# Optimization experiments

Hardware: AMD Instinct MI355X
Metric: run time of the kernel (lower is better)

The kernel has to match this reference:

```python
import jax, jax.numpy as jnp
import numpy as np

B, N, C = 8, 2048, 512
CR = C // 8  # reduced channels = int(channels * 1/8) = 64


def setup_inputs() -> dict:
    key = jax.random.key(0)
    ks = jax.random.split(key, 8)
    s = 0.02
    return {
        "x": jax.random.normal(ks[0], (B, N, C), dtype=jnp.float32),
        "Wk": jax.random.normal(ks[1], (CR, C), dtype=jnp.float32) * s,
        "bk": jax.random.normal(ks[2], (CR,), dtype=jnp.float32) * s,
        "Wv": jax.random.normal(ks[3], (CR, C), dtype=jnp.float32) * s,
        "bv": jax.random.normal(ks[4], (CR,), dtype=jnp.float32) * s,
        "Wq": jax.random.normal(ks[5], (C, C), dtype=jnp.float32) * s,
        "bq": jax.random.normal(ks[6], (C,), dtype=jnp.float32) * s,
        "gamma": jax.random.normal(ks[7], (1,), dtype=jnp.float32),
    }


def reference(x, Wk, bk, Wv, bv, Wq, bq, gamma):
    # x: [B, N, C]; flat_x in torch is x.transpose(1,2) -> [B, C, N]
    fx = jnp.transpose(x, (0, 2, 1))  # [B, C, N]
    # conv1d kernel_size=1 == channel projection
    k = jnp.einsum('oc,bcn->bno', Wk, fx) + bk            # [B, N, CR] (already transposed)
    v = jnp.einsum('oc,bcn->bon', Wv, fx) + bv[:, None]   # [B, CR, N]
    kv = jnp.einsum('bnc,bcm->bnm', k, v)                 # [B, N, N]
    att = jax.nn.softmax(kv, axis=1)                      # softmax over dim=1 as in torch
    q = jnp.einsum('oc,bcn->bon', Wq, fx) + bq[:, None]   # [B, C, N]
    refined = jnp.einsum('bcn,bnm->bcm', q, att)          # [B, C, N]
    refined = jnp.transpose(refined, (0, 2, 1))           # back to [B, N, C]
    return gamma * refined + x
```

## Files before the change

kernel.cpp:

```cpp
#include <hip/hip_runtime.h>

typedef __attribute__((ext_vector_type(4))) float f32x4;
typedef __attribute__((ext_vector_type(8))) __bf16 bf16x8;
typedef __attribute__((ext_vector_type(8))) unsigned short u16x8;

__device__ __forceinline__ unsigned short f2bf(float f) {
  unsigned u = __builtin_bit_cast(unsigned, f);
  u += 0x7fffu + ((u >> 16) & 1u);
  return (unsigned short)(u >> 16);
}
__device__ __forceinline__ unsigned pack2bf(float lo, float hi) {
  return (unsigned)f2bf(lo) | ((unsigned)f2bf(hi) << 16);
}
__device__ __forceinline__ u16x8 cvt8(float4 a, float4 b) {
  u16x8 h;
  h[0] = f2bf(a.x); h[1] = f2bf(a.y); h[2] = f2bf(a.z); h[3] = f2bf(a.w);
  h[4] = f2bf(b.x); h[5] = f2bf(b.y); h[6] = f2bf(b.z); h[7] = f2bf(b.w);
  return h;
}
__device__ __forceinline__ bf16x8 frag_at(const unsigned short* p) {
  return *reinterpret_cast<const bf16x8*>(p);
}
__device__ __forceinline__ f32x4 mfma16(bf16x8 a, bf16x8 b, f32x4 c) {
  return __builtin_amdgcn_mfma_f32_16x16x32_bf16(a, b, c, 0, 0, 0);
}

__global__ __launch_bounds__(512, 2) void proj_all_kernel(
    const float* __restrict__ x,
    const float* __restrict__ Wk, const float* __restrict__ bk,
    const float* __restrict__ Wv, const float* __restrict__ bv,
    const float* __restrict__ Wq, const float* __restrict__ bq,
    unsigned short* __restrict__ kbf, unsigned short* __restrict__ vtbf,
    unsigned short* __restrict__ qt) {
  __shared__ unsigned short As[256][72];
  __shared__ unsigned short Bs[128][72];
  const int t = threadIdx.x;
  const int w = t >> 6, lane = t & 63, lr = lane & 15, lg = lane >> 4;

  if (blockIdx.x < 128) {
    const int tok0 = blockIdx.x * 128;
    const int tr = w & 3, oh = w >> 2;
    f32x4 acc[2][4];
#pragma unroll
    for (int a = 0; a < 2; ++a)
#pragma unroll
      for (int c = 0; c < 4; ++c) acc[a][c] = (f32x4){0.f, 0.f, 0.f, 0.f};

    for (int kk = 0; kk < 8; ++kk) {
      const int k0 = kk * 64;
      {
        int row = t >> 2, q = t & 3;
        const float4* src = reinterpret_cast<const float4*>(
            x + (size_t)(tok0 + row) * 512 + k0 + q * 16);
        float4 f0 = src[0], f1 = src[1], f2 = src[2], f3 = src[3];
        *reinterpret_cast<u16x8*>(&As[row][q * 16])     = cvt8(f0, f1);
        *reinterpret_cast<u16x8*>(&As[row][q * 16 + 8]) = cvt8(f2, f3);
      }
      {
        int row = t >> 2, q = t & 3;
        const float* wsrc = (row < 64) ? (Wk + (size_t)row * 512)
                                       : (Wv + (size_t)(row - 64) * 512);
        const float4* src = reinterpret_cast<const float4*>(wsrc + k0 + q * 16);
        float4 f0 = src[0], f1 = src[1], f2 = src[2], f3 = src[3];
        *reinterpret_cast<u16x8*>(&Bs[row][q * 16])     = cvt8(f0, f1);
        *reinterpret_cast<u16x8*>(&Bs[row][q * 16 + 8]) = cvt8(f2, f3);
      }
      __syncthreads();
#pragma unroll
      for (int s = 0; s < 2; ++s) {
        bf16x8 af[2];
#pragma unroll
        for (int tb = 0; tb < 2; ++tb)
          af[tb] = frag_at(&As[tr * 32 + tb * 16 + lr][s * 32 + lg * 8]);
#pragma unroll
        for (int ob = 0; ob < 4; ++ob) {
          bf16x8 bfr = frag_at(&Bs[oh * 64 + ob * 16 + lr][s * 32 + lg * 8]);
#pragma unroll
          for (int tb = 0; tb < 2; ++tb)
            acc[tb][ob] = mfma16(af[tb], bfr, acc[tb][ob]);
        }
      }
      __syncthreads();
    }
#pragma unroll
    for (int ob = 0; ob < 4; ++ob) {
      const int o = oh * 64 + ob * 16 + lr;
      const float bias = (o < 64) ? bk[o] : bv[o - 64];
#pragma unroll
      for (int tb = 0; tb < 2; ++tb)
#pragma unroll
        for (int i = 0; i < 4; ++i) {
          const int token = tok0 + tr * 32 + tb * 16 + lg * 4 + i;
          const unsigned short hv = f2bf(acc[tb][ob][i] + bias);
          if (o < 64) kbf[(size_t)token * 64 + o] = hv;
          else        vtbf[(size_t)token * 64 + (o - 64)] = hv;
        }
    }
  } else {
    const int bi = blockIdx.x - 128;
    const int b = bi & 7, r = bi >> 3, ot = r >> 4, ntl = r & 15;
    const int o0 = ot * 256, n0 = ntl * 128;
    const int orr = w & 3, nh = w >> 2;
    f32x4 acc[4][4];
#pragma unroll
    for (int a = 0; a < 4; ++a)
#pragma unroll
      for (int c = 0; c < 4; ++c) acc[a][c] = (f32x4){0.f, 0.f, 0.f, 0.f};

    for (int kk = 0; kk < 8; ++kk) {
      const int k0 = kk * 64;
      {
        int row = t >> 1, h = t & 1;
        const float4* src = reinterpret_cast<const float4*>(
            Wq + (size_t)(o0 + row) * 512 + k0 + h * 32);
        float4 f0 = src[0], f1 = src[1];
        *reinterpret_cast<u16x8*>(&As[row][h * 32]) = cvt8(f0, f1);
        float4 f2 = src[2], f3 = src[3];
        *reinterpret_cast<u16x8*>(&As[row][h * 32 + 8]) = cvt8(f2, f3);
        float4 f4 = src[4], f5 = src[5];
        *reinterpret_cast<u16x8*>(&As[row][h * 32 + 16]) = cvt8(f4, f5);
        float4 f6 = src[6], f7 = src[7];
        *reinterpret_cast<u16x8*>(&As[row][h * 32 + 24]) = cvt8(f6, f7);
      }
      {
        int row = t >> 2, q = t & 3;
        const float4* src = reinterpret_cast<const float4*>(
            x + ((size_t)b * 2048 + n0 + row) * 512 + k0 + q * 16);
        float4 f0 = src[0], f1 = src[1], f2 = src[2], f3 = src[3];
        *reinterpret_cast<u16x8*>(&Bs[row][q * 16])     = cvt8(f0, f1);
        *reinterpret_cast<u16x8*>(&Bs[row][q * 16 + 8]) = cvt8(f2, f3);
      }
      __syncthreads();
#pragma unroll
      for (int s = 0; s < 2; ++s) {
        bf16x8 bfr[4];
#pragma unroll
        for (int nb = 0; nb < 4; ++nb)
          bfr[nb] = frag_at(&Bs[nh * 64 + nb * 16 + lr][s * 32 + lg * 8]);
#pragma unroll
        for (int ob = 0; ob < 4; ++ob) {
          bf16x8 af = frag_at(&As[orr * 64 + ob * 16 + lr][s * 32 + lg * 8]);
#pragma unroll
          for (int nb = 0; nb < 4; ++nb)
            acc[ob][nb] = mfma16(af, bfr[nb], acc[ob][nb]);
        }
      }
      __syncthreads();
    }
#pragma unroll
    for (int ob = 0; ob < 4; ++ob)
#pragma unroll
      for (int i = 0; i < 4; ++i) {
        const int o = o0 + orr * 64 + ob * 16 + lg * 4 + i;
        const float bias = bq[o];
#pragma unroll
        for (int nb = 0; nb < 4; ++nb) {
          const int n = n0 + nh * 64 + nb * 16 + lr;
          qt[((size_t)b * 512 + o) * 2048 + n] = f2bf(acc[ob][nb][i] + bias);
        }
      }
  }
}

__global__ __launch_bounds__(256, 2) void attn_kernel(
    const float* __restrict__ x, const unsigned short* __restrict__ kbf,
    const unsigned short* __restrict__ vtbf, const unsigned short* __restrict__ qt,
    const float* __restrict__ g, float* __restrict__ out) {
  __shared__ unsigned short p_lds[2][64][72];
  __shared__ float dsum_lds[64];
  const int t = threadIdx.x;
  const int b = blockIdx.x & 7;
  const int rest = blockIdx.x >> 3;
  const int mt = rest >> 1, ch = rest & 1;
  const int m0 = mt * 64;
  const int w = t >> 6, lane = t & 63, lr = lane & 15, lg = lane >> 4;

  const unsigned short* kbase = kbf + (size_t)b * 2048 * 64;
  const unsigned short* vrow =
      vtbf + (size_t)(b * 2048 + m0 + w * 16 + lr) * 64;
  const bf16x8 qf0 = frag_at(vrow + lg * 8);
  const bf16x8 qf1 = frag_at(vrow + 32 + lg * 8);
  const unsigned short* qtb = qt + ((size_t)b * 512 + ch * 256 + w * 64) * 2048;

  f32x4 acc[4][4];
#pragma unroll
  for (int mc = 0; mc < 4; ++mc)
#pragma unroll
    for (int cb = 0; cb < 4; ++cb) acc[mc][cb] = (f32x4){0.f, 0.f, 0.f, 0.f};
  float dsum = 0.f;

  bf16x8 kf[4][2], bfr[4][2];
#pragma unroll
  for (int nb = 0; nb < 4; ++nb) {
    const unsigned short* krow = kbase + (size_t)(nb * 16 + lr) * 64;
    kf[nb][0] = frag_at(krow + lg * 8);
    kf[nb][1] = frag_at(krow + 32 + lg * 8);
  }
#pragma unroll
  for (int cb = 0; cb < 4; ++cb) {
    const unsigned short* qrow = qtb + (size_t)(cb * 16 + lr) * 2048;
    bfr[cb][0] = frag_at(qrow + lg * 8);
    bfr[cb][1] = frag_at(qrow + 32 + lg * 8);
  }

  for (int nt = 0; nt < 32; ++nt) {
    const int buf = nt & 1;
    const int nn = ((nt + 1) & 31) * 64;

    f32x4 sacc[4];
#pragma unroll
    for (int nb = 0; nb < 4; ++nb) {
      sacc[nb] = (f32x4){0.f, 0.f, 0.f, 0.f};
      sacc[nb] = mfma16(kf[nb][0], qf0, sacc[nb]);
      sacc[nb] = mfma16(kf[nb][1], qf1, sacc[nb]);
    }
#pragma unroll
    for (int nb = 0; nb < 4; ++nb) {
      const unsigned short* krow = kbase + (size_t)(nn + nb * 16 + lr) * 64;
      kf[nb][0] = frag_at(krow + lg * 8);
      kf[nb][1] = frag_at(krow + 32 + lg * 8);
    }
#pragma unroll
    for (int nb = 0; nb < 4; ++nb) {
      float e0 = __expf(sacc[nb][0]);
      float e1 = __expf(sacc[nb][1]);
      float e2 = __expf(sacc[nb][2]);
      float e3 = __expf(sacc[nb][3]);
      dsum += (e0 + e1) + (e2 + e3);
      uint2 pk;
      pk.x = pack2bf(e0, e1);
      pk.y = pack2bf(e2, e3);
      *reinterpret_cast<uint2*>(&p_lds[buf][w * 16 + lr][nb * 16 + lg * 4]) = pk;
    }
    __syncthreads();

#pragma unroll
    for (int mc = 0; mc < 4; ++mc) {
      bf16x8 pf0 = frag_at(&p_lds[buf][mc * 16 + lr][lg * 8]);
      bf16x8 pf1 = frag_at(&p_lds[buf][mc * 16 + lr][32 + lg * 8]);
#pragma unroll
      for (int cb = 0; cb < 4; ++cb) {
        acc[mc][cb] = mfma16(pf0, bfr[cb][0], acc[mc][cb]);
        acc[mc][cb] = mfma16(pf1, bfr[cb][1], acc[mc][cb]);
      }
    }
#pragma unroll
    for (int cb = 0; cb < 4; ++cb) {
      const unsigned short* qrow = qtb + (size_t)(cb * 16 + lr) * 2048 + nn;
      bfr[cb][0] = frag_at(qrow + lg * 8);
      bfr[cb][1] = frag_at(qrow + 32 + lg * 8);
    }
  }

  dsum += __shfl_xor(dsum, 16);
  dsum += __shfl_xor(dsum, 32);
  if (lane < 16) dsum_lds[w * 16 + lane] = dsum;
  __syncthreads();

  const float gamma = g[0];
#pragma unroll
  for (int mc = 0; mc < 4; ++mc) {
#pragma unroll
    for (int i = 0; i < 4; ++i) {
      const int mrow = mc * 16 + lg * 4 + i;
      const float s = gamma / dsum_lds[mrow];
      const size_t base =
          ((size_t)b * 2048 + m0 + mrow) * 512 + ch * 256 + w * 64;
#pragma unroll
      for (int cb = 0; cb < 4; ++cb) {
        const size_t idx = base + cb * 16 + lr;
        out[idx] = acc[mc][cb][i] * s + x[idx];
      }
    }
  }
}

extern "C" void kernel_launch(void* const* d_in, const int* in_sizes, int n_in,
                              void* d_out, int out_size, void* d_ws, size_t ws_size,
                              hipStream_t stream) {
  const float* x  = (const float*)d_in[0];
  const float* Wk = (const float*)d_in[1];
  const float* bk = (const float*)d_in[2];
  const float* Wv = (const float*)d_in[3];
  const float* bv = (const float*)d_in[4];
  const float* Wq = (const float*)d_in[5];
  const float* bq = (const float*)d_in[6];
  const float* g  = (const float*)d_in[7];
  float* out = (float*)d_out;

  char* ws = (char*)d_ws;
  unsigned short* kbf  = (unsigned short*)(ws);
  unsigned short* vtbf = (unsigned short*)(ws + 2097152);
  unsigned short* qt   = (unsigned short*)(ws + 4194304);

  hipLaunchKernelGGL(proj_all_kernel, dim3(384), dim3(512), 0, stream,
                     x, Wk, bk, Wv, bv, Wq, bq, kbf, vtbf, qt);
  hipLaunchKernelGGL(attn_kernel, dim3(512), dim3(256), 0, stream,
                     x, kbf, vtbf, qt, g, out);
}
```

Before: 250.1 us.

## Shrink projection and attention tiles to double grid size and raise occupancy

```diff
diff --git a/kernel.cpp b/kernel.cpp
--- a/kernel.cpp
+++ b/kernel.cpp
@@ -1,22 +1,18 @@
 #include <hip/hip_runtime.h>
 
 typedef __attribute__((ext_vector_type(4))) float f32x4;
+typedef __attribute__((ext_vector_type(4))) __bf16 bf16x4;
 typedef __attribute__((ext_vector_type(8))) __bf16 bf16x8;
 typedef __attribute__((ext_vector_type(8))) unsigned short u16x8;
 
 __device__ __forceinline__ unsigned short f2bf(float f) {
-  unsigned u = __builtin_bit_cast(unsigned, f);
-  u += 0x7fffu + ((u >> 16) & 1u);
-  return (unsigned short)(u >> 16);
-}
-__device__ __forceinline__ unsigned pack2bf(float lo, float hi) {
-  return (unsigned)f2bf(lo) | ((unsigned)f2bf(hi) << 16);
+  __bf16 h = (__bf16)f;
+  return __builtin_bit_cast(unsigned short, h);
 }
 __device__ __forceinline__ u16x8 cvt8(float4 a, float4 b) {
-  u16x8 h;
-  h[0] = f2bf(a.x); h[1] = f2bf(a.y); h[2] = f2bf(a.z); h[3] = f2bf(a.w);
-  h[4] = f2bf(b.x); h[5] = f2bf(b.y); h[6] = f2bf(b.z); h[7] = f2bf(b.w);
-  return h;
+  bf16x8 h = {(__bf16)a.x, (__bf16)a.y, (__bf16)a.z, (__bf16)a.w,
+              (__bf16)b.x, (__bf16)b.y, (__bf16)b.z, (__bf16)b.w};
+  return __builtin_bit_cast(u16x8, h);
 }
 __device__ __forceinline__ bf16x8 frag_at(const unsigned short* p) {
   return *reinterpret_cast<const bf16x8*>(p);
@@ -25,73 +21,67 @@
   return __builtin_amdgcn_mfma_f32_16x16x32_bf16(a, b, c, 0, 0, 0);
 }
 
-__global__ __launch_bounds__(512, 2) void proj_all_kernel(
+__global__ __launch_bounds__(512, 4) void proj_all_kernel(
     const float* __restrict__ x,
     const float* __restrict__ Wk, const float* __restrict__ bk,
     const float* __restrict__ Wv, const float* __restrict__ bv,
     const float* __restrict__ Wq, const float* __restrict__ bq,
     unsigned short* __restrict__ kbf, unsigned short* __restrict__ vtbf,
     unsigned short* __restrict__ qt) {
-  __shared__ unsigned short As[256][72];
+  __shared__ unsigned short As[128][72];
   __shared__ unsigned short Bs[128][72];
   const int t = threadIdx.x;
   const int w = t >> 6, lane = t & 63, lr = lane & 15, lg = lane >> 4;
+  const int wr = w >> 2, wc = w & 3;
+  const int srow = t >> 2, sq = t & 3;
+
+  f32x4 acc[4][2];
+#pragma unroll
+  for (int a = 0; a < 4; ++a)
+#pragma unroll
+    for (int c = 0; c < 2; ++c) acc[a][c] = (f32x4){0.f, 0.f, 0.f, 0.f};
 
   if (blockIdx.x < 128) {
     const int tok0 = blockIdx.x * 128;
-    const int tr = w & 3, oh = w >> 2;
-    f32x4 acc[2][4];
-#pragma unroll
-    for (int a = 0; a < 2; ++a)
-#pragma unroll
-      for (int c = 0; c < 4; ++c) acc[a][c] = (f32x4){0.f, 0.f, 0.f, 0.f};
-
+    const float* wrow = (srow < 64) ? (Wk + (size_t)srow * 512)
+                                    : (Wv + (size_t)(srow - 64) * 512);
     for (int kk = 0; kk < 8; ++kk) {
       const int k0 = kk * 64;
       {
-        int row = t >> 2, q = t & 3;
-        const float4* src = reinterpret_cast<const float4*>(
-            x + (size_t)(tok0 + row) * 512 + k0 + q * 16);
-        float4 f0 = src[0], f1 = src[1], f2 = src[2], f3 = src[3];
-        *reinterpret_cast<u16x8*>(&As[row][q * 16])     = cvt8(f0, f1);
-        *reinterpret_cast<u16x8*>(&As[row][q * 16 + 8]) = cvt8(f2, f3);
-      }
-      {
-        int row = t >> 2, q = t & 3;
-        const float* wsrc = (row < 64) ? (Wk + (size_t)row * 512)
-                                       : (Wv + (size_t)(row - 64) * 512);
-        const float4* src = reinterpret_cast<const float4*>(wsrc + k0 + q * 16);
-        float4 f0 = src[0], f1 = src[1], f2 = src[2], f3 = src[3];
-        *reinterpret_cast<u16x8*>(&Bs[row][q * 16])     = cvt8(f0, f1);
-        *reinterpret_cast<u16x8*>(&Bs[row][q * 16 + 8]) = cvt8(f2, f3);
+        const float4* sa = reinterpret_cast<const float4*>(
+            x + (size_t)(tok0 + srow) * 512 + k0 + sq * 16);
+        float4 a0 = sa[0], a1 = sa[1], a2 = sa[2], a3 = sa[3];
+        *reinterpret_cast<u16x8*>(&As[srow][sq * 16])     = cvt8(a0, a1);
+        *reinterpret_cast<u16x8*>(&As[srow][sq * 16 + 8]) = cvt8(a2, a3);
+        const float4* sb = reinterpret_cast<const float4*>(wrow + k0 + sq * 16);
+        float4 b0 = sb[0], b1 = sb[1], b2 = sb[2], b3 = sb[3];
+        *reinterpret_cast<u16x8*>(&Bs[srow][sq * 16])     = cvt8(b0, b1);
+        *reinterpret_cast<u16x8*>(&Bs[srow][sq * 16 + 8]) = cvt8(b2, b3);
       }
       __syncthreads();
 #pragma unroll
       for (int s = 0; s < 2; ++s) {
-        bf16x8 af[2];
-#pragma unroll
-        for (int tb = 0; tb < 2; ++tb)
-          af[tb] = frag_at(&As[tr * 32 + tb * 16 + lr][s * 32 + lg * 8]);
-#pragma unroll
-        for (int ob = 0; ob < 4; ++ob) {
-          bf16x8 bfr = frag_at(&Bs[oh * 64 + ob * 16 + lr][s * 32 + lg * 8]);
-#pragma unroll
-          for (int tb = 0; tb < 2; ++tb)
-            acc[tb][ob] = mfma16(af[tb], bfr, acc[tb][ob]);
-        }
-      }
-      __syncthreads();
-    }
-#pragma unroll
-    for (int ob = 0; ob < 4; ++ob) {
-      const int o = oh * 64 + ob * 16 + lr;
+        bf16x8 bf0 = frag_at(&Bs[wc * 32 + lr][s * 32 + lg * 8]);
+        bf16x8 bf1 = frag_at(&Bs[wc * 32 + 16 + lr][s * 32 + lg * 8]);
+#pragma unroll
+        for (int ab = 0; ab < 4; ++ab) {
+          bf16x8 af = frag_at(&As[wr * 64 + ab * 16 + lr][s * 32 + lg * 8]);
+          acc[ab][0] = mfma16(af, bf0, acc[ab][0]);
+          acc[ab][1] = mfma16(af, bf1, acc[ab][1]);
+        }
+      }
+      __syncthreads();
+    }
+#pragma unroll
+    for (int nb = 0; nb < 2; ++nb) {
+      const int o = wc * 32 + nb * 16 + lr;
       const float bias = (o < 64) ? bk[o] : bv[o - 64];
 #pragma unroll
-      for (int tb = 0; tb < 2; ++tb)
+      for (int ab = 0; ab < 4; ++ab)
 #pragma unroll
         for (int i = 0; i < 4; ++i) {
-          const int token = tok0 + tr * 32 + tb * 16 + lg * 4 + i;
-          const unsigned short hv = f2bf(acc[tb][ob][i] + bias);
+          const int token = tok0 + wr * 64 + ab * 16 + lg * 4 + i;
+          const unsigned short hv = f2bf(acc[ab][nb][i] + bias);
           if (o < 64) kbf[(size_t)token * 64 + o] = hv;
           else        vtbf[(size_t)token * 64 + (o - 64)] = hv;
         }
@@ -99,70 +89,51 @@
   } else {
     const int bi = blockIdx.x - 128;
     const int b = bi & 7, r = bi >> 3, ot = r >> 4, ntl = r & 15;
-    const int o0 = ot * 256, n0 = ntl * 128;
-    const int orr = w & 3, nh = w >> 2;
-    f32x4 acc[4][4];
-#pragma unroll
-    for (int a = 0; a < 4; ++a)
-#pragma unroll
-      for (int c = 0; c < 4; ++c) acc[a][c] = (f32x4){0.f, 0.f, 0.f, 0.f};
-
+    const int o0 = ot * 128, n0 = ntl * 128;
     for (int kk = 0; kk < 8; ++kk) {
       const int k0 = kk * 64;
       {
-        int row = t >> 1, h = t & 1;
-        const float4* src = reinterpret_cast<const float4*>(
-            Wq + (size_t)(o0 + row) * 512 + k0 + h * 32);
-        float4 f0 = src[0], f1 = src[1];
-        *reinterpret_cast<u16x8*>(&As[row][h * 32]) = cvt8(f0, f1);
-        float4 f2 = src[2], f3 = src[3];
-        *reinterpret_cast<u16x8*>(&As[row][h * 32 + 8]) = cvt8(f2, f3);
-        float4 f4 = src[4], f5 = src[5];
-        *reinterpret_cast<u16x8*>(&As[row][h * 32 + 16]) = cvt8(f4, f5);
-        float4 f6 = src[6], f7 = src[7];
-        *reinterpret_cast<u16x8*>(&As[row][h * 32 + 24]) = cvt8(f6, f7);
-      }
-      {
-        int row = t >> 2, q = t & 3;
-        const float4* src = reinterpret_cast<const float4*>(
-            x + ((size_t)b * 2048 + n0 + row) * 512 + k0 + q * 16);
-        float4 f0 = src[0], f1 = src[1], f2 = src[2], f3 = src[3];
-        *reinterpret_cast<u16x8*>(&Bs[row][q * 16])     = cvt8(f0, f1);
-        *reinterpret_cast<u16x8*>(&Bs[row][q * 16 + 8]) = cvt8(f2, f3);
+        const float4* sa = reinterpret_cast<const float4*>(
+            Wq + (size_t)(o0 + srow) * 512 + k0 + sq * 16);
+        float4 a0 = sa[0], a1 = sa[1], a2 = sa[2], a3 = sa[3];
+        *reinterpret_cast<u16x8*>(&As[srow][sq * 16])     = cvt8(a0, a1);
+        *reinterpret_cast<u16x8*>(&As[srow][sq * 16 + 8]) = cvt8(a2, a3);
+        const float4* sb = reinterpret_cast<const float4*>(
+            x + ((size_t)b * 2048 + n0 + srow) * 512 + k0 + sq * 16);
+        float4 b0 = sb[0], b1 = sb[1], b2 = sb[2], b3 = sb[3];
+        *reinterpret_cast<u16x8*>(&Bs[srow][sq * 16])     = cvt8(b0, b1);
+        *reinterpret_cast<u16x8*>(&Bs[srow][sq * 16 + 8]) = cvt8(b2, b3);
       }
       __syncthreads();
 #pragma unroll
       for (int s = 0; s < 2; ++s) {
-        bf16x8 bfr[4];
-#pragma unroll
-        for (int nb = 0; nb < 4; ++nb)
-          bfr[nb] = frag_at(&Bs[nh * 64 + nb * 16 + lr][s * 32 + lg * 8]);
-#pragma unroll
-        for (int ob = 0; ob < 4; ++ob) {
-          bf16x8 af = frag_at(&As[orr * 64 + ob * 16 + lr][s * 32 + lg * 8]);
-#pragma unroll
-          for (int nb = 0; nb < 4; ++nb)
-            acc[ob][nb] = mfma16(af, bfr[nb], acc[ob][nb]);
-        }
-      }
-      __syncthreads();
-    }
-#pragma unroll
-    for (int ob = 0; ob < 4; ++ob)
+        bf16x8 bf0 = frag_at(&Bs[wc * 32 + lr][s * 32 + lg * 8]);
+        bf16x8 bf1 = frag_at(&Bs[wc * 32 + 16 + lr][s * 32 + lg * 8]);
+#pragma unroll
+        for (int ab = 0; ab < 4; ++ab) {
+          bf16x8 af = frag_at(&As[wr * 64 + ab * 16 + lr][s * 32 + lg * 8]);
+          acc[ab][0] = mfma16(af, bf0, acc[ab][0]);
+          acc[ab][1] = mfma16(af, bf1, acc[ab][1]);
+        }
+      }
+      __syncthreads();
+    }
+#pragma unroll
+    for (int ab = 0; ab < 4; ++ab)
 #pragma unroll
       for (int i = 0; i < 4; ++i) {
-        const int o = o0 + orr * 64 + ob * 16 + lg * 4 + i;
+        const int o = o0 + wr * 64 + ab * 16 + lg * 4 + i;
         const float bias = bq[o];
 #pragma unroll
-        for (int nb = 0; nb < 4; ++nb) {
-          const int n = n0 + nh * 64 + nb * 16 + lr;
-          qt[((size_t)b * 512 + o) * 2048 + n] = f2bf(acc[ob][nb][i] + bias);
-        }
-      }
-  }
-}
-
-__global__ __launch_bounds__(256, 2) void attn_kernel(
+        for (int nb = 0; nb < 2; ++nb) {
+          const int n = n0 + wc * 32 + nb * 16 + lr;
+          qt[((size_t)b * 512 + o) * 2048 + n] = f2bf(acc[ab][nb][i] + bias);
+        }
+      }
+  }
+}
+
+__global__ __launch_bounds__(256, 4) void attn_kernel(
     const float* __restrict__ x, const unsigned short* __restrict__ kbf,
     const unsigned short* __restrict__ vtbf, const unsigned short* __restrict__ qt,
     const float* __restrict__ g, float* __restrict__ out) {
@@ -171,7 +142,7 @@
   const int t = threadIdx.x;
   const int b = blockIdx.x & 7;
   const int rest = blockIdx.x >> 3;
-  const int mt = rest >> 1, ch = rest & 1;
+  const int mt = rest >> 2, ch = rest & 3;
   const int m0 = mt * 64;
   const int w = t >> 6, lane = t & 63, lr = lane & 15, lg = lane >> 4;
 
@@ -180,16 +151,17 @@
       vtbf + (size_t)(b * 2048 + m0 + w * 16 + lr) * 64;
   const bf16x8 qf0 = frag_at(vrow + lg * 8);
   const bf16x8 qf1 = frag_at(vrow + 32 + lg * 8);
-  const unsigned short* qtb = qt + ((size_t)b * 512 + ch * 256 + w * 64) * 2048;
-
-  f32x4 acc[4][4];
+  const unsigned short* qtb =
+      qt + ((size_t)b * 512 + ch * 128 + w * 32) * 2048;
+
+  f32x4 acc[4][2];
 #pragma unroll
   for (int mc = 0; mc < 4; ++mc)
 #pragma unroll
-    for (int cb = 0; cb < 4; ++cb) acc[mc][cb] = (f32x4){0.f, 0.f, 0.f, 0.f};
+    for (int cb = 0; cb < 2; ++cb) acc[mc][cb] = (f32x4){0.f, 0.f, 0.f, 0.f};
   float dsum = 0.f;
 
-  bf16x8 kf[4][2], bfr[4][2];
+  bf16x8 kf[4][2], bfr[2][2];
 #pragma unroll
   for (int nb = 0; nb < 4; ++nb) {
     const unsigned short* krow = kbase + (size_t)(nb * 16 + lr) * 64;
@@ -197,7 +169,7 @@
     kf[nb][1] = frag_at(krow + 32 + lg * 8);
   }
 #pragma unroll
-  for (int cb = 0; cb < 4; ++cb) {
+  for (int cb = 0; cb < 2; ++cb) {
     const unsigned short* qrow = qtb + (size_t)(cb * 16 + lr) * 2048;
     bfr[cb][0] = frag_at(qrow + lg * 8);
     bfr[cb][1] = frag_at(qrow + 32 + lg * 8);
@@ -205,7 +177,6 @@
 
   for (int nt = 0; nt < 32; ++nt) {
     const int buf = nt & 1;
-    const int nn = ((nt + 1) & 31) * 64;
 
     f32x4 sacc[4];
 #pragma unroll
@@ -214,11 +185,14 @@
       sacc[nb] = mfma16(kf[nb][0], qf0, sacc[nb]);
       sacc[nb] = mfma16(kf[nb][1], qf1, sacc[nb]);
     }
-#pragma unroll
-    for (int nb = 0; nb < 4; ++nb) {
-      const unsigned short* krow = kbase + (size_t)(nn + nb * 16 + lr) * 64;
-      kf[nb][0] = frag_at(krow + lg * 8);
-      kf[nb][1] = frag_at(krow + 32 + lg * 8);
+    if (nt + 1 < 32) {
+#pragma unroll
+      for (int nb = 0; nb < 4; ++nb) {
+        const unsigned short* krow =
+            kbase + (size_t)((nt + 1) * 64 + nb * 16 + lr) * 64;
+        kf[nb][0] = frag_at(krow + lg * 8);
+        kf[nb][1] = frag_at(krow + 32 + lg * 8);
+      }
     }
 #pragma unroll
     for (int nb = 0; nb < 4; ++nb) {
@@ -227,28 +201,31 @@
       float e2 = __expf(sacc[nb][2]);
       float e3 = __expf(sacc[nb][3]);
       dsum += (e0 + e1) + (e2 + e3);
-      uint2 pk;
-      pk.x = pack2bf(e0, e1);
-      pk.y = pack2bf(e2, e3);
-      *reinterpret_cast<uint2*>(&p_lds[buf][w * 16 + lr][nb * 16 + lg * 4]) = pk;
-    }
-    __syncthreads();
+      bf16x4 pk = {(__bf16)e0, (__bf16)e1, (__bf16)e2, (__bf16)e3};
+      *reinterpret_cast<bf16x4*>(&p_lds[buf][w * 16 + lr][nb * 16 + lg * 4]) = pk;
+    }
+    asm volatile("s_waitcnt lgkmcnt(0)" ::: "memory");
+    __builtin_amdgcn_s_barrier();
+    asm volatile("" ::: "memory");
 
 #pragma unroll
     for (int mc = 0; mc < 4; ++mc) {
       bf16x8 pf0 = frag_at(&p_lds[buf][mc * 16 + lr][lg * 8]);
       bf16x8 pf1 = frag_at(&p_lds[buf][mc * 16 + lr][32 + lg * 8]);
 #pragma unroll
-      for (int cb = 0; cb < 4; ++cb) {
+      for (int cb = 0; cb < 2; ++cb) {
         acc[mc][cb] = mfma16(pf0, bfr[cb][0], acc[mc][cb]);
         acc[mc][cb] = mfma16(pf1, bfr[cb][1], acc[mc][cb]);
       }
     }
-#pragma unroll
-    for (int cb = 0; cb < 4; ++cb) {
-      const unsigned short* qrow = qtb + (size_t)(cb * 16 + lr) * 2048 + nn;
-      bfr[cb][0] = frag_at(qrow + lg * 8);
-      bfr[cb][1] = frag_at(qrow + 32 + lg * 8);
+    if (nt + 1 < 32) {
+#pragma unroll
+      for (int cb = 0; cb < 2; ++cb) {
+        const unsigned short* qrow =
+            qtb + (size_t)(cb * 16 + lr) * 2048 + (nt + 1) * 64;
+        bfr[cb][0] = frag_at(qrow + lg * 8);
+        bfr[cb][1] = frag_at(qrow + 32 + lg * 8);
+      }
     }
   }
 
@@ -265,9 +242,9 @@
       const int mrow = mc * 16 + lg * 4 + i;
       const float s = gamma / dsum_lds[mrow];
       const size_t base =
-          ((size_t)b * 2048 + m0 + mrow) * 512 + ch * 256 + w * 64;
-#pragma unroll
-      for (int cb = 0; cb < 4; ++cb) {
+          ((size_t)b * 2048 + m0 + mrow) * 512 + ch * 128 + w * 32;
+#pragma unroll
+      for (int cb = 0; cb < 2; ++cb) {
         const size_t idx = base + cb * 16 + lr;
         out[idx] = acc[mc][cb][i] * s + x[idx];
       }
@@ -293,8 +270,8 @@
   unsigned short* vtbf = (unsigned short*)(ws + 2097152);
   unsigned short* qt   = (unsigned short*)(ws + 4194304);
 
-  hipLaunchKernelGGL(proj_all_kernel, dim3(384), dim3(512), 0, stream,
+  hipLaunchKernelGGL(proj_all_kernel, dim3(640), dim3(512), 0, stream,
                      x, Wk, bk, Wv, bv, Wq, bq, kbf, vtbf, qt);
-  hipLaunchKernelGGL(attn_kernel, dim3(512), dim3(256), 0, stream,
+  hipLaunchKernelGGL(attn_kernel, dim3(1024), dim3(256), 0, stream,
                      x, kbf, vtbf, qt, g, out);
 }
```

Result: slower. 295.2 us (+18.0%).
